# Performance work log

Measured on AMD Instinct MI355X. Metric: run time of the kernel, lower is better.

Reference implementation:

```python
import jax, jax.numpy as jnp
import numpy as np

# ---- static config matching init_kwargs / input_specs ----
B, H, W_IN, IN_CAPS, ATOMS = 2, 48, 48, 8, 16
KER, STRIDE, OUT_CAPS, ROUTINGS = 3, 1, 16, 3


def setup_inputs() -> dict:
    key = jax.random.key(0)
    k1, k2 = jax.random.split(key)
    x = jax.random.normal(k1, (B, H, W_IN, IN_CAPS * (ATOMS + 1)), dtype=jnp.float32)
    # W: [input_num_capsule, num_capsule, 4, 4], he_normal-ish scale (fan_in=16)
    W = jax.random.normal(k2, (IN_CAPS, OUT_CAPS, 4, 4), dtype=jnp.float32) * np.float32((2.0 / 16.0) ** 0.5)
    return {"input_tensor": x, "W": W}


def _kernel_tile(x, k=KER, stride=STRIDE):
    # Equivalent to the depthwise-conv patch-extraction trick + transpose:
    # output [B, Ho, Wo, k*k, C]
    b, h, w, c = x.shape
    ho = (h - k) // stride + 1
    wo = (w - k) // stride + 1
    patches = jnp.stack(
        [x[:, i:i + stride * ho:stride, j:j + stride * wo:stride, :]
         for i in range(k) for j in range(k)],
        axis=3,
    )
    return patches


def _squash(s, eps=1e-7):
    sq = jnp.sum(s * s, axis=-1, keepdims=True)
    return (sq / (1.0 + sq)) * s / jnp.sqrt(sq + eps)


def reference(input_tensor, W):
    t = _kernel_tile(input_tensor)                      # [B,Ho,Wo,kk,C]
    b, ho, wo, kk, c = t.shape
    n = b * ho * wo
    t = t.reshape(n, kk * IN_CAPS, ATOMS + 1)           # [N, kk*in_caps, 17]
    pose = t[..., :ATOMS].reshape(n, kk, IN_CAPS, 4, 4)
    act = t[..., ATOMS].reshape(n, kk * IN_CAPS)        # input capsule activations
    # vote transform: pose @ W per (input capsule -> output capsule)
    votes = jnp.einsum('nkiab,iobc->nkioac', pose, W)
    votes = votes.reshape(n, kk * IN_CAPS, OUT_CAPS, ATOMS)  # [N, kkin, out, 16]
    # iterative routing-by-agreement, weighted by input activation
    logits = jnp.zeros((n, kk * IN_CAPS, OUT_CAPS), dtype=votes.dtype)
    v = None
    for r in range(ROUTINGS):
        coup = jax.nn.softmax(logits, axis=2) * act[:, :, None]
        s = jnp.einsum('nko,nkoe->noe', coup, votes)    # weighted vote sum
        v = _squash(s)                                  # [N, out, 16]
        if r < ROUTINGS - 1:
            logits = logits + jnp.einsum('nkoe,noe->nko', votes, v)
    return v.reshape(b, ho, wo, OUT_CAPS, ATOMS)
```

## Files before the change

kernel.cpp:

```cpp
#include <hip/hip_runtime.h>


#define IN_CAPS 8
#define OUT_CAPS 16
#define KK 9
#define KKIN 72
#define BATCH 2
#define H_IN 48
#define W_IN 48
#define HO 46
#define WO 46
#define CIN 136
#define NPIX (BATCH*HO*WO)

template<int CTRL>
__device__ __forceinline__ float dpp_f(float x) {
    return __int_as_float(
        __builtin_amdgcn_update_dpp(0, __float_as_int(x), CTRL, 0xF, 0xF, true));
}
__device__ __forceinline__ float row_sum16(float x) {
    x += dpp_f<0xB1>(x);
    x += dpp_f<0x4E>(x);
    x += dpp_f<0x124>(x);
    x += dpp_f<0x128>(x);
    return x;
}

__global__ __launch_bounds__(256, 4)
void capsule_routing_kernel(const float* __restrict__ x,
                            const float* __restrict__ Wg,
                            float* __restrict__ out)
{
    __shared__ alignas(16) float pose_s[KKIN * 20];
    __shared__ alignas(16) float pose_t[16 * 76];
    __shared__ float act_s[KKIN];
    __shared__ alignas(16) float wg_s[IN_CAPS*OUT_CAPS*20];
    __shared__ alignas(16) float coup_s[OUT_CAPS * 76];
    __shared__ alignas(16) float logits_s[KKIN * 20];

    const int tid = threadIdx.x;
    const int o = tid >> 4;
    const int e = tid & 15;
    const int c = e & 3;

    const int n   = blockIdx.x;
    const int b   = n / (HO * WO);
    const int rem = n - b * (HO * WO);
    const int ho  = rem / WO;
    const int wo  = rem - ho * WO;

    for (int i = tid; i < IN_CAPS * OUT_CAPS * 16; i += 256) wg_s[i] = Wg[i];

    for (int idx = tid; idx < KK * CIN; idx += 256) {
        int p  = idx / CIN;
        int cc = idx - p * CIN;
        int py = p / 3, px = p - py * 3;
        float val = x[(((b * H_IN + ho + py) * W_IN) + (wo + px)) * CIN + cc];
        int ic = cc / 17;
        int aa = cc - ic * 17;
        int k  = p * IN_CAPS + ic;
        if (aa == 16) {
            act_s[k] = val;
        } else {
            pose_s[k * 20 + aa] = val;
            pose_t[aa * 76 + k] = val;
        }
    }
    __syncthreads();

    float wreg[IN_CAPS][4], wreg2[IN_CAPS][4];
    #pragma unroll
    for (int i = 0; i < IN_CAPS; ++i) {
        #pragma unroll
        for (int bb = 0; bb < 4; ++bb)
            wreg[i][bb] = wg_s[((i * OUT_CAPS + o) * 4 + bb) * 4 + c];
        const float4 wr = *reinterpret_cast<const float4*>(
            &wg_s[((i * OUT_CAPS + o) * 4 + c) * 4]);
        wreg2[i][0] = wr.x; wreg2[i][1] = wr.y; wreg2[i][2] = wr.z; wreg2[i][3] = wr.w;
    }

    if (tid < KKIN) {
        float cv = act_s[tid] * 0.0625f;
        #pragma unroll
        for (int j = 0; j < OUT_CAPS; ++j) coup_s[j * 76 + tid] = cv;
    }
    __syncthreads();

    const int kbase = tid >> 4;
    const int od    = tid & 15;
    const int icd   = kbase & 7;
    float lreg[5] = {0.f, 0.f, 0.f, 0.f, 0.f};

    const float4* cp = reinterpret_cast<const float4*>(&coup_s[o * 76]);
    const float4* pp = reinterpret_cast<const float4*>(&pose_t[e * 76]);

    float v = 0.f;
    #pragma unroll 1
    for (int r = 0; r < 3; ++r) {
        float M[8] = {0.f,0.f,0.f,0.f,0.f,0.f,0.f,0.f};
        #pragma unroll
        for (int p = 0; p < KK; ++p) {
            const float4 c0 = cp[2*p], c1 = cp[2*p+1];
            const float4 p0 = pp[2*p], p1 = pp[2*p+1];
            M[0] = fmaf(c0.x, p0.x, M[0]);
            M[1] = fmaf(c0.y, p0.y, M[1]);
            M[2] = fmaf(c0.z, p0.z, M[2]);
            M[3] = fmaf(c0.w, p0.w, M[3]);
            M[4] = fmaf(c1.x, p1.x, M[4]);
            M[5] = fmaf(c1.y, p1.y, M[5]);
            M[6] = fmaf(c1.z, p1.z, M[6]);
            M[7] = fmaf(c1.w, p1.w, M[7]);
        }
        float s0 = 0.f, s1 = 0.f, s2 = 0.f, s3 = 0.f;
        #pragma unroll
        for (int ic = 0; ic < 8; ++ic) {
            s0 = fmaf(wreg[ic][0], dpp_f<0x00>(M[ic]), s0);
            s1 = fmaf(wreg[ic][1], dpp_f<0x55>(M[ic]), s1);
            s2 = fmaf(wreg[ic][2], dpp_f<0xAA>(M[ic]), s2);
            s3 = fmaf(wreg[ic][3], dpp_f<0xFF>(M[ic]), s3);
        }
        const float s = (s0 + s1) + (s2 + s3);

        const float sq = row_sum16(s * s);
        v = s * (sq / ((1.f + sq) * sqrtf(sq + 1e-7f)));

        if (r < 2) {
            const float vq0 = dpp_f<0x00>(v);
            const float vq1 = dpp_f<0x55>(v);
            const float vq2 = dpp_f<0xAA>(v);
            const float vq3 = dpp_f<0xFF>(v);
            #pragma unroll
            for (int ic = 0; ic < 8; ++ic) {
                float g = wreg2[ic][0] * vq0 + wreg2[ic][1] * vq1
                        + wreg2[ic][2] * vq2 + wreg2[ic][3] * vq3;
                wg_s[(ic * OUT_CAPS + o) * 20 + e] = g;
            }
            __syncthreads();
            const float4* gp = reinterpret_cast<const float4*>(
                &wg_s[(icd * OUT_CAPS + od) * 20]);
            const float4 g0 = gp[0], g1 = gp[1], g2 = gp[2], g3 = gp[3];
            #pragma unroll
            for (int j = 0; j < 5; ++j) {
                const int k = kbase + 16 * j;
                if (k < KKIN) {
                    const float4* pk = reinterpret_cast<const float4*>(&pose_s[k * 20]);
                    const float4 p0 = pk[0], p1 = pk[1], p2 = pk[2], p3 = pk[3];
                    float d0 = p0.x*g0.x + p0.y*g0.y + p0.z*g0.z + p0.w*g0.w;
                    float d1 = p1.x*g1.x + p1.y*g1.y + p1.z*g1.z + p1.w*g1.w;
                    float d2 = p2.x*g2.x + p2.y*g2.y + p2.z*g2.z + p2.w*g2.w;
                    float d3 = p3.x*g3.x + p3.y*g3.y + p3.z*g3.z + p3.w*g3.w;
                    lreg[j] += (d0 + d1) + (d2 + d3);
                    logits_s[k * 20 + od] = lreg[j];
                }
            }
            __syncthreads();
            if (tid < 2 * KKIN) {
                const int k  = tid >> 1;
                const int hf = tid & 1;
                const float4* lp = reinterpret_cast<const float4*>(
                    &logits_s[k * 20 + hf * 8]);
                const float4 l0 = lp[0], l1 = lp[1];
                float lg[8] = {l0.x,l0.y,l0.z,l0.w, l1.x,l1.y,l1.z,l1.w};
                float mx = -1e30f;
                #pragma unroll
                for (int j = 0; j < 8; ++j) mx = fmaxf(mx, lg[j]);
                mx = fmaxf(mx, dpp_f<0xB1>(mx));
                float sum = 0.f;
                #pragma unroll
                for (int j = 0; j < 8; ++j) { lg[j] = __expf(lg[j] - mx); sum += lg[j]; }
                sum += dpp_f<0xB1>(sum);
                const float scale = act_s[k] / sum;
                #pragma unroll
                for (int j = 0; j < 8; ++j) coup_s[(hf * 8 + j) * 76 + k] = lg[j] * scale;
            }
            __syncthreads();
        }
    }

    out[n * 256 + tid] = v;
}

extern "C" void kernel_launch(void* const* d_in, const int* in_sizes, int n_in,
                              void* d_out, int out_size, void* d_ws, size_t ws_size,
                              hipStream_t stream) {
    const float* x  = (const float*)d_in[0];
    const float* Wt = (const float*)d_in[1];
    float* outp = (float*)d_out;
    capsule_routing_kernel<<<dim3(NPIX), dim3(256), 0, stream>>>(x, Wt, outp);
}
```

Measured before the change: 98.49 us.

## Fuse logit update into softmax threads and pad shared rows against bank conflicts

The logit-update dot products are remapped so that each of 144 threads computes the 8 logits it later softmaxes, keeping them in registers. This removes the logits_s shared buffer and one __syncthreads per routing iteration. The pose and g rows in shared memory get skewed padding to reduce bank conflicts. In exchange, only 144 of 256 threads do that dot-product work, each now computing 8 dot products instead of up to 5.

Result: slower. 115.0 us (+16.7%).

```diff
diff --git a/kernel.cpp b/kernel.cpp
--- a/kernel.cpp
+++ b/kernel.cpp
@@ -26,17 +26,23 @@
     return x;
 }
 
+__device__ __forceinline__ int pose_row(int k) {
+    return k * 20 + ((k >> 3) & 1) * 4;
+}
+__device__ __forceinline__ int g_row(int o, int ic) {
+    return (o * 8 + ic) * 20 + o * 4;
+}
+
 __global__ __launch_bounds__(256, 4)
 void capsule_routing_kernel(const float* __restrict__ x,
                             const float* __restrict__ Wg,
                             float* __restrict__ out)
 {
-    __shared__ alignas(16) float pose_s[KKIN * 20];
+    __shared__ alignas(16) float pose_s[1440];
     __shared__ alignas(16) float pose_t[16 * 76];
     __shared__ float act_s[KKIN];
-    __shared__ alignas(16) float wg_s[IN_CAPS*OUT_CAPS*20];
+    __shared__ alignas(16) float wg_s[2620];
     __shared__ alignas(16) float coup_s[OUT_CAPS * 76];
-    __shared__ alignas(16) float logits_s[KKIN * 20];
 
     const int tid = threadIdx.x;
     const int o = tid >> 4;
@@ -62,7 +68,7 @@
         if (aa == 16) {
             act_s[k] = val;
         } else {
-            pose_s[k * 20 + aa] = val;
+            pose_s[pose_row(k) + aa] = val;
             pose_t[aa * 76 + k] = val;
         }
     }
@@ -86,10 +92,10 @@
     }
     __syncthreads();
 
-    const int kbase = tid >> 4;
-    const int od    = tid & 15;
-    const int icd   = kbase & 7;
-    float lreg[5] = {0.f, 0.f, 0.f, 0.f, 0.f};
+    const int kf  = tid >> 1;
+    const int hf  = tid & 1;
+    const int ick = kf & 7;
+    float lreg8[8] = {0.f,0.f,0.f,0.f,0.f,0.f,0.f,0.f};
 
     const float4* cp = reinterpret_cast<const float4*>(&coup_s[o * 76]);
     const float4* pp = reinterpret_cast<const float4*>(&pose_t[e * 76]);
@@ -133,34 +139,27 @@
             for (int ic = 0; ic < 8; ++ic) {
                 float g = wreg2[ic][0] * vq0 + wreg2[ic][1] * vq1
                         + wreg2[ic][2] * vq2 + wreg2[ic][3] * vq3;
-                wg_s[(ic * OUT_CAPS + o) * 20 + e] = g;
+                wg_s[g_row(o, ic) + e] = g;
             }
             __syncthreads();
-            const float4* gp = reinterpret_cast<const float4*>(
-                &wg_s[(icd * OUT_CAPS + od) * 20]);
-            const float4 g0 = gp[0], g1 = gp[1], g2 = gp[2], g3 = gp[3];
-            #pragma unroll
-            for (int j = 0; j < 5; ++j) {
-                const int k = kbase + 16 * j;
-                if (k < KKIN) {
-                    const float4* pk = reinterpret_cast<const float4*>(&pose_s[k * 20]);
-                    const float4 p0 = pk[0], p1 = pk[1], p2 = pk[2], p3 = pk[3];
+            if (tid < 2 * KKIN) {
+                const float4* pk = reinterpret_cast<const float4*>(
+                    &pose_s[pose_row(kf)]);
+                const float4 p0 = pk[0], p1 = pk[1], p2 = pk[2], p3 = pk[3];
+                float lg[8];
+                #pragma unroll
+                for (int j = 0; j < 8; ++j) {
+                    const int oo = hf * 8 + j;
+                    const float4* gp = reinterpret_cast<const float4*>(
+                        &wg_s[g_row(oo, ick)]);
+                    const float4 g0 = gp[0], g1 = gp[1], g2 = gp[2], g3 = gp[3];
                     float d0 = p0.x*g0.x + p0.y*g0.y + p0.z*g0.z + p0.w*g0.w;
                     float d1 = p1.x*g1.x + p1.y*g1.y + p1.z*g1.z + p1.w*g1.w;
                     float d2 = p2.x*g2.x + p2.y*g2.y + p2.z*g2.z + p2.w*g2.w;
                     float d3 = p3.x*g3.x + p3.y*g3.y + p3.z*g3.z + p3.w*g3.w;
-                    lreg[j] += (d0 + d1) + (d2 + d3);
-                    logits_s[k * 20 + od] = lreg[j];
+                    lreg8[j] += (d0 + d1) + (d2 + d3);
+                    lg[j] = lreg8[j];
                 }
-            }
-            __syncthreads();
-            if (tid < 2 * KKIN) {
-                const int k  = tid >> 1;
-                const int hf = tid & 1;
-                const float4* lp = reinterpret_cast<const float4*>(
-                    &logits_s[k * 20 + hf * 8]);
-                const float4 l0 = lp[0], l1 = lp[1];
-                float lg[8] = {l0.x,l0.y,l0.z,l0.w, l1.x,l1.y,l1.z,l1.w};
                 float mx = -1e30f;
                 #pragma unroll
                 for (int j = 0; j < 8; ++j) mx = fmaxf(mx, lg[j]);
@@ -169,9 +168,10 @@
                 #pragma unroll
                 for (int j = 0; j < 8; ++j) { lg[j] = __expf(lg[j] - mx); sum += lg[j]; }
                 sum += dpp_f<0xB1>(sum);
-                const float scale = act_s[k] / sum;
+                const float scale = act_s[kf] / sum;
                 #pragma unroll
-                for (int j = 0; j < 8; ++j) coup_s[(hf * 8 + j) * 76 + k] = lg[j] * scale;
+                for (int j = 0; j < 8; ++j)
+                    coup_s[(hf * 8 + j) * 76 + kf] = lg[j] * scale;
             }
             __syncthreads();
         }
```
